# Performance work log

Hardware: AMD Instinct MI355X
Metric: run time of the kernel (lower is better)

The kernel has to match this reference:

```python
import jax, jax.numpy as jnp
import numpy as np

NUM_ANCHORS = 32
MAX_DIST = 3
DDE_ROUNDS = 2
DDE_REV_ROUNDS = 2
PE_ANCHOR_DIM = 16


def setup_inputs() -> dict:
    key = jax.random.key(0)
    ks = jax.random.split(key, 20)
    N, Ntext, NT, E, R, D, H = 20000, 19500, 500, 200000, 500, 256, 256
    PE = DDE_ROUNDS + DDE_REV_ROUNDS + PE_ANCHOR_DIM + 3
    s = 0.02
    return {
        "h_ids": jax.random.randint(ks[0], (E,), 0, N),
        "r_ids": jax.random.randint(ks[1], (E,), 0, R),
        "t_ids": jax.random.randint(ks[2], (E,), 0, N),
        "q_emb": jax.random.normal(ks[3], (D,), jnp.float32),
        "entity_embs": jax.random.normal(ks[4], (Ntext, D), jnp.float32),
        "relation_embs": jax.random.normal(ks[5], (R, D), jnp.float32),
        "topic_entity_ids": jax.random.randint(ks[6], (4,), 0, N),
        "num_entities": N,
        "num_non_text_entities": NT,
        "non_text_emb": jax.random.normal(ks[7], (1, D)) * s,
        "dist_emb": jax.random.normal(ks[8], (MAX_DIST + 2, PE_ANCHOR_DIM)) * s,
        "W_enc": jax.random.normal(ks[9], (D + PE, H)) * s,
        "b_enc": jnp.zeros((H,)),
        "gnn_W_msg": jax.random.normal(ks[10], (2, H + D, H)) * s,
        "gnn_W_gate": jax.random.normal(ks[11], (2, 2 * H, H)) * s,
        "gnn_W_upd": jax.random.normal(ks[12], (2, H, H)) * s,
        "W_out": jax.random.normal(ks[13], (H, D)) * s,
        "scorer_W1": jax.random.normal(ks[14], (4 * D + 4, H)) * s,
        "scorer_b1": jnp.zeros((H,)),
        "scorer_W2": jax.random.normal(ks[15], (H, 1)) * s,
        "scorer_b2": jnp.zeros((1,)),
    }


def reference(h_ids, r_ids, t_ids, q_emb, entity_embs, relation_embs,
              topic_entity_ids, num_entities, num_non_text_entities,
              non_text_emb, dist_emb, W_enc, b_enc,
              gnn_W_msg, gnn_W_gate, gnn_W_upd, W_out,
              scorer_W1, scorer_b1, scorer_W2, scorer_b2):
    N = num_entities
    D = q_emb.shape[0]
    E = h_ids.shape[0]
    # assemble all entity embeddings (text + broadcast non-text)
    all_emb = jnp.concatenate(
        [entity_embs, jnp.broadcast_to(non_text_emb, (num_non_text_entities, D))], axis=0)
    # anchor triple selection: question-conditioned triple scores, top-k
    qe = all_emb @ q_emb            # [N]
    qr = relation_embs @ q_emb      # [R]
    tri_score = qe[h_ids] + qr[r_ids] + qe[t_ids]  # [E]
    anchor_scores, anchor_idx = jax.lax.top_k(tri_score, NUM_ANCHORS)
    # topic DDE positional encoding (mean-aggregated label propagation)
    topic = jnp.zeros((N,), all_emb.dtype).at[topic_entity_ids].set(1.0)
    deg_t = jnp.maximum(jnp.zeros((N,)).at[t_ids].add(1.0), 1.0)
    deg_h = jnp.maximum(jnp.zeros((N,)).at[h_ids].add(1.0), 1.0)
    cols = []
    s = topic
    for _ in range(DDE_ROUNDS):
        s = jnp.zeros((N,)).at[t_ids].add(s[h_ids]) / deg_t
        cols.append(s)
    s = topic
    for _ in range(DDE_REV_ROUNDS):
        s = jnp.zeros((N,)).at[h_ids].add(s[t_ids]) / deg_h
        cols.append(s)
    pe_topic = jnp.stack(cols, axis=1)  # [N, 4]
    # anchor proximity PE: bounded BFS distance, embedded
    anchor_mask = (jnp.zeros((N,)).at[h_ids[anchor_idx]].set(1.0)
                   .at[t_ids[anchor_idx]].set(1.0))
    FAR = float(MAX_DIST + 1)
    dist = jnp.where(anchor_mask > 0, 0.0, FAR)
    for _ in range(MAX_DIST):
        c1 = jnp.full((N,), FAR).at[t_ids].min(dist[h_ids] + 1.0)
        c2 = jnp.full((N,), FAR).at[h_ids].min(dist[t_ids] + 1.0)
        dist = jnp.minimum(dist, jnp.minimum(c1, c2))
    pe_anchor = dist_emb[dist.astype(jnp.int32)]  # [N, 16]
    # path indicators (topic flag, anchor-endpoint flag, subgraph mask = full graph)
    path_ind = jnp.stack([topic, anchor_mask, jnp.ones((N,))], axis=1)
    pe_full = jnp.concatenate([pe_topic, pe_anchor, path_ind], axis=1)  # [N, 23]
    # gated GNN refine over the (full) anchor subgraph
    h = jax.nn.relu(jnp.concatenate([all_emb, pe_full], axis=1) @ W_enc + b_enc)
    rel_e = relation_embs[r_ids]  # [E, D]
    for l in range(gnn_W_msg.shape[0]):
        msg = jax.nn.relu(jnp.concatenate([h[h_ids], rel_e], axis=1) @ gnn_W_msg[l])
        agg = jnp.zeros_like(h).at[t_ids].add(msg)
        gate = jax.nn.sigmoid(jnp.concatenate([h, agg], axis=1) @ gnn_W_gate[l])
        h = h + gate * jnp.tanh(agg @ gnn_W_upd[l])
    h_final = h @ W_out  # back to emb_dim, assembled over all entities
    # scalar triple features
    is_anchor = jnp.zeros((E,)).at[anchor_idx].set(1.0)
    a_score = jnp.zeros((E,)).at[anchor_idx].set(jax.lax.stop_gradient(anchor_scores))
    scalar_feats = jnp.stack([is_anchor, a_score, topic[h_ids], topic[t_ids]], axis=1)
    # triple scorer MLP
    feats = jnp.concatenate([
        jnp.broadcast_to(q_emb, (E, D)), h_final[h_ids], rel_e,
        h_final[t_ids], scalar_feats], axis=1)  # [E, 4D+4]
    hid = jax.nn.relu(feats @ scorer_W1 + scorer_b1)
    return (hid @ scorer_W2 + scorer_b2)[:, 0]
```

## Files before the change

### kernel.cpp

```cpp
#include <hip/hip_runtime.h>
#include <math.h>

#define CDIV(a,b) (((a)+(b)-1)/(b))

typedef short short8 __attribute__((ext_vector_type(8)));
typedef float f32x4  __attribute__((ext_vector_type(4)));
typedef unsigned short u16;

__device__ __forceinline__ float warp_sum(float v){
  #pragma unroll
  for (int o=32;o;o>>=1) v += __shfl_down(v,o);
  return v;
}
__device__ __forceinline__ int warp_min(int v){
  #pragma unroll
  for (int o=32;o;o>>=1) v = min(v,__shfl_down(v,o));
  return v;
}
__device__ __forceinline__ u16 f2bf(float f){
  unsigned u = __float_as_uint(f);
  unsigned r = 0x7fffu + ((u>>16)&1u);
  return (u16)((u + r)>>16);
}
__device__ __forceinline__ float bl(u16 v){ return __uint_as_float(((unsigned)v)<<16); }

__global__ __launch_bounds__(256)
void k_rowdot_all(const float* __restrict__ ent, const float* __restrict__ nontext,
                  const float* __restrict__ q, float* __restrict__ qe,
                  int N, int Ntext,
                  const float* __restrict__ rel, float* __restrict__ qr, int R, int nb1){
  int wid = threadIdx.x>>6, lane = threadIdx.x&63;
  const float* src; float* dst; int row;
  if ((int)blockIdx.x < nb1){
    row = blockIdx.x*4 + wid; if (row >= N) return;
    src = (row < Ntext) ? (ent + (size_t)row*256) : nontext;
    dst = qe;
  } else {
    row = (blockIdx.x-nb1)*4 + wid; if (row >= R) return;
    src = rel + (size_t)row*256;
    dst = qr;
  }
  float4 a = *(const float4*)(src + lane*4);
  float4 b = *(const float4*)(q + lane*4);
  float s = a.x*b.x + a.y*b.y + a.z*b.z + a.w*b.w;
  s = warp_sum(s);
  if (!lane) dst[row] = s;
}

__global__ __launch_bounds__(256)
void k_tri(const int* __restrict__ h, const int* __restrict__ r,
           const int* __restrict__ t, const float* __restrict__ qe,
           const float* __restrict__ qr, float* __restrict__ tri,
           float* __restrict__ bmax, int* __restrict__ degh, int* __restrict__ degi, int E){
  __shared__ float red[256];
  int e = blockIdx.x*256 + threadIdx.x;
  float v = -INFINITY;
  if (e < E){
    int hh=h[e], rr=r[e], tt=t[e];
    v = qe[hh] + qr[rr] + qe[tt];
    tri[e] = v;
    atomicAdd(&degh[hh], 1);
    atomicAdd(&degi[tt], 1);
  }
  red[threadIdx.x]=v; __syncthreads();
  for (int s=128;s;s>>=1){ if ((int)threadIdx.x<s) red[threadIdx.x]=fmaxf(red[threadIdx.x],red[threadIdx.x+s]); __syncthreads(); }
  if (!threadIdx.x) bmax[blockIdx.x]=red[0];
}

__global__ __launch_bounds__(64)
void k_thresh(const float* __restrict__ bmax, float* __restrict__ thrT, int nb){
  int lane = threadIdx.x;
  float m = -INFINITY;
  for (int i=lane; i<nb; i+=64) m = fmaxf(m, bmax[i]);
  for (int it=0; it<32; it++){
    float bv = m; int bln = lane;
    #pragma unroll
    for (int o=32;o;o>>=1){
      float ov = __shfl_down(bv,o);
      int   ol = __shfl_down(bln,o);
      if (ov>bv){ bv=ov; bln=ol; }
    }
    float mv = __shfl(bv,0);
    int   wl = __shfl(bln,0);
    if (lane==wl) m = -INFINITY;
    if (it==31 && lane==0) thrT[0]=mv;
  }
}

__global__ void k_compact(const float* __restrict__ tri, const float* __restrict__ thrT,
                          int* __restrict__ cnt, int* __restrict__ ci, float* __restrict__ cv, int E){
  int e = blockIdx.x*256 + threadIdx.x; if (e>=E) return;
  float v = tri[e];
  if (v >= thrT[0]){
    int p = atomicAdd(cnt, 1);
    ci[p]=e; cv[p]=v;
  }
}

__global__ __launch_bounds__(64)
void k_final32(const int* __restrict__ ci, const float* __restrict__ cv, const int* __restrict__ cnt,
               int* __restrict__ ai, float* __restrict__ as,
               const int* __restrict__ h_ids, const int* __restrict__ t_ids,
               const int* __restrict__ topicId, int nTopic,
               float* __restrict__ topic, float* __restrict__ amask){
  int lane = threadIdx.x;
  int C = *cnt; if (C > 1024) C = 1024;
  int nIter = CDIV(C,64);
  unsigned selMask = 0;
  int myai=0; float myas=0.f;
  for (int it=0; it<32; it++){
    float bv=-INFINITY; int bi=0x7fffffff; int bj=-1;
    for (int j=0;j<nIter;j++){
      int p = lane + j*64;
      if (p < C && !((selMask>>j)&1u)){
        float v = cv[p]; int idx = ci[p];
        if (v>bv || (v==bv && idx<bi)){ bv=v; bi=idx; bj=j; }
      }
    }
    int bln = lane;
    #pragma unroll
    for (int o=32;o;o>>=1){
      float ov=__shfl_down(bv,o); int oi=__shfl_down(bi,o);
      int   oj=__shfl_down(bj,o); int ol=__shfl_down(bln,o);
      if (ov>bv || (ov==bv && oi<bi)){ bv=ov; bi=oi; bj=oj; bln=ol; }
    }
    float wv=__shfl(bv,0); int wi=__shfl(bi,0);
    int   wj=__shfl(bj,0); int wl=__shfl(bln,0);
    if (lane==wl) selMask |= (1u<<wj);
    if (lane==it){ myai=wi; myas=wv; }
  }
  if (lane<32){
    ai[lane]=myai; as[lane]=myas;
    int e = myai;
    amask[h_ids[e]]=1.f;
    amask[t_ids[e]]=1.f;
  }
  if (lane<nTopic) topic[topicId[lane]]=1.f;
}

__global__ void k_scan1(const int* __restrict__ degT, const int* __restrict__ degH,
                        int* __restrict__ offsT, int* __restrict__ offsH,
                        int* __restrict__ bsum, int N, int nb){
  __shared__ int s[256];
  int which = (int)blockIdx.x >= nb;
  int b = which ? blockIdx.x - nb : blockIdx.x;
  const int* deg = which ? degH : degT;
  int* offs = which ? offsH : offsT;
  int i = b*256 + threadIdx.x;
  int v = (i<N) ? deg[i] : 0;
  s[threadIdx.x] = v; __syncthreads();
  #pragma unroll
  for (int o=1;o<256;o<<=1){
    int add = (threadIdx.x>=(unsigned)o) ? s[threadIdx.x-o] : 0; __syncthreads();
    s[threadIdx.x] += add; __syncthreads();
  }
  if (i<N) offs[i] = s[threadIdx.x] - v;
  if (threadIdx.x==255) bsum[blockIdx.x] = s[255];
}
__global__ void k_scan2two(int* __restrict__ bsum, int nb){
  __shared__ int s[256];
  int t=threadIdx.x;
  int half = t>>7, idx = t&127;
  int v = (idx<nb)? bsum[half*nb+idx] : 0;
  s[t]=v; __syncthreads();
  #pragma unroll
  for (int o=1;o<128;o<<=1){ int add=(idx>=o)?s[t-o]:0; __syncthreads(); s[t]+=add; __syncthreads(); }
  if (idx<nb) bsum[half*nb+idx] = s[t]-v;
}
__global__ void k_scan3(int* __restrict__ offsT, int* __restrict__ offsH,
                        const int* __restrict__ bsum,
                        int* __restrict__ curT, int* __restrict__ curH, int N, int nb){
  int which = (int)blockIdx.x >= nb;
  int b = which ? blockIdx.x - nb : blockIdx.x;
  int i = b*256+threadIdx.x; if (i>=N) return;
  int* offs = which ? offsH : offsT;
  int* cur  = which ? curH  : curT;
  int o = offs[i] + bsum[blockIdx.x];
  offs[i]=o; cur[i]=o;
}
__global__ void k_place(const int* __restrict__ h, const int* __restrict__ r,
                        const int* __restrict__ t,
                        int* __restrict__ curT, int* __restrict__ curH,
                        int4* __restrict__ ehr4, int* __restrict__ etH, int E){
  int e = blockIdx.x*256+threadIdx.x; if (e>=E) return;
  int hh=h[e], tt=t[e];
  int pos = atomicAdd(&curT[tt], 1);
  ehr4[pos] = make_int4(hh, r[e], e, 0);
  int posh = atomicAdd(&curH[hh], 1);
  etH[posh] = tt;
}

__global__ __launch_bounds__(256)
void k_dde2(const int* __restrict__ offsT, const int* __restrict__ degT, const int4* __restrict__ ehr4,
            const int* __restrict__ offsH, const int* __restrict__ degH, const int* __restrict__ etH,
            const float* __restrict__ s0, const float* __restrict__ s1,
            float* __restrict__ sn0, float* __restrict__ sn1,
            float* __restrict__ pe4, int c0, int c1,
            const float* __restrict__ amask, int* __restrict__ dist0, int N){
  int wid=threadIdx.x>>6, lane=threadIdx.x&63;
  int i = blockIdx.x*4+wid; if (i>=N) return;
  int dir = blockIdx.y;
  const int* offs = dir ? offsH : offsT;
  const int* deg  = dir ? degH  : degT;
  const float* s  = dir ? s1 : s0;
  float* sn       = dir ? sn1 : sn0;
  int col         = dir ? c1 : c0;
  int start=offs[i], cnt=deg[i];
  float a=0.f;
  if (dir){
    for (int k=lane;k<cnt;k+=64) a += s[etH[start+k]];
  } else {
    for (int k=lane;k<cnt;k+=64) a += s[ehr4[start+k].x];
  }
  a = warp_sum(a);
  if (!lane){
    float v = a / fmaxf((float)cnt,1.f);
    if (sn) sn[i]=v;
    pe4[i*4+col]=v;
    if (dist0 && !dir) dist0[i] = (amask[i]>0.f)?0:4;
  }
}

__global__ __launch_bounds__(256)
void k_bfs_g(const int* __restrict__ offsT, const int* __restrict__ degT, const int4* __restrict__ ehr4,
             const int* __restrict__ offsH, const int* __restrict__ degH, const int* __restrict__ etH,
             const int* __restrict__ din, int* __restrict__ dout, int N){
  int wid=threadIdx.x>>6, lane=threadIdx.x&63;
  int i = blockIdx.x*4+wid; if (i>=N) return;
  int sT=offsT[i], cT=degT[i];
  int sH=offsH[i], cH=degH[i];
  int best = 4;
  for (int k=lane;k<cT;k+=64) best = min(best, din[ehr4[sT+k].x]+1);
  for (int k=lane;k<cH;k+=64) best = min(best, din[etH[sH+k]]+1);
  best = warp_min(best);
  if (!lane) dout[i] = min(din[i], best);
}

__global__ void k_smalls(const float* __restrict__ dist_e, const float* __restrict__ W_enc,
                         float* __restrict__ distW,
                         const float* __restrict__ nontext, float* __restrict__ encnt,
                         const float* __restrict__ q, const float* __restrict__ W1,
                         const float* __restrict__ b1, float* __restrict__ bias2){
  int b = blockIdx.x, j = threadIdx.x;
  if (b < 5){
    const float* Wpe = W_enc + (256+4)*256;
    float s=0.f;
    #pragma unroll
    for (int p=0;p<16;p++) s += dist_e[b*16+p]*Wpe[p*256+j];
    distW[b*256+j]=s;
  } else if (b == 5){
    float s=0.f;
    for (int k=0;k<256;k++) s += nontext[k]*W_enc[k*256+j];
    encnt[j]=s;
  } else {
    float s=b1[j];
    for (int k=0;k<256;k++) s += q[k]*W1[k*256+j];
    bias2[j]=s;
  }
}

__global__ __launch_bounds__(64)
void k_packall(const float* __restrict__ W_enc, const float* __restrict__ W_msg,
               const float* __restrict__ W_gate, const float* __restrict__ W_upd,
               const float* __restrict__ W1, u16* __restrict__ pbAll){
  int f = blockIdx.x, lane = threadIdx.x;
  int tgt, fid, nt16;
  if      (f < 128) { tgt=0; fid=f;      nt16=16; }
  else if (f < 256) { tgt=1; fid=f-128;  nt16=16; }
  else if (f < 384) { tgt=2; fid=f-256;  nt16=16; }
  else if (f < 896) { tgt=3; fid=f-384;  nt16=32; }
  else if (f < 1408){ tgt=4; fid=f-896;  nt16=32; }
  else if (f < 1792){ tgt=5; fid=f-1408; nt16=48; }
  else              { tgt=6; fid=f-1792; nt16=32; }
  int ks = fid/nt16, nt = fid%nt16;
  int kb = ks*32 + 8*(lane>>4);
  int n  = nt*16 + (lane&15);
  u16 v[8];
  #pragma unroll
  for (int i=0;i<8;i++){
    int k = kb+i;
    float x;
    if (tgt==0) x = W_enc[(size_t)k*256+n];
    else if (tgt==1) x = W_msg[(size_t)k*256+n];
    else if (tgt==2) x = W_msg[(size_t)(512+k)*256+n];
    else if (tgt==3 || tgt==4){
      const float* Wg = W_gate + (tgt==4 ? (size_t)512*256 : 0);
      const float* Wu = W_upd  + (tgt==4 ? (size_t)256*256 : 0);
      int blk = n>>4, c = ((blk>>1)<<4) | (n&15);
      if ((blk&1)==0) x = Wg[(size_t)k*256+c];
      else            x = (k<256) ? 0.f : Wu[(size_t)(k-256)*256+c];
    }
    else if (tgt==5){
      if (n<256)      x = W_msg[(size_t)(256+k)*256+n];
      else if (n<512) x = W_msg[(size_t)(768+k)*256+(n-256)];
      else            x = W1[(size_t)(512+k)*256+(n-512)];
    } else {
      if (n<256) x = W1[(size_t)(256+k)*256+n];
      else       x = W1[(size_t)(768+k)*256+(n-256)];
    }
    v[i]=f2bf(x);
  }
  *(uint4*)(pbAll + ((size_t)f*64+lane)*8) = *(uint4*)v;
}

__global__ __launch_bounds__(64)
void k_packf32(const float* __restrict__ W, u16* __restrict__ Bp){
  int f = blockIdx.x, lane = threadIdx.x;
  int ks = f/32, nt = f%32;
  int kb = ks*32 + 8*(lane>>4);
  int n  = nt*16 + (lane&15);
  u16 v[8];
  #pragma unroll
  for (int i=0;i<8;i++) v[i] = f2bf(W[(size_t)(kb+i)*512 + n]);
  *(uint4*)(Bp + ((size_t)f*64+lane)*8) = *(uint4*)v;
}

template<int NCOLS, int CT, int MODE, bool AF32, int MR>
__global__ __launch_bounds__(256)
void k_bgemm(const float* __restrict__ A1f, const u16* __restrict__ A2a,
             const u16* __restrict__ A2b, int K1,
             const u16* __restrict__ Bp, void* __restrict__ Cout,
             const float* __restrict__ xb, const float* __restrict__ W_enc,
             const float* __restrict__ pe4, const int* __restrict__ dist,
             const float* __restrict__ topic, const float* __restrict__ amask,
             const float* __restrict__ distW,
             int M, int K)
{
  constexpr int NT16 = NCOLS/16;
  constexpr int CPB  = NCOLS/CT;
  constexpr int NREP = CPB/32;
  const int tid  = threadIdx.x;
  const int lane = tid & 63;
  const int w    = tid >> 6;
  const int wr   = w >> 1, wc = w & 1;
  const int ct   = blockIdx.y;
  const int row0 = (blockIdx.x*2 + wr)*(16*MR);
  const int lrow = lane & 15;
  const int kc   = lane >> 4;
  int arow[MR];
  #pragma unroll
  for (int m=0;m<MR;m++){
    int rr = row0 + m*16 + lrow;
    arow[m] = (rr >= M) ? M-1 : rr;
  }

  f32x4 acc[MR][NREP];
  #pragma unroll
  for (int m=0;m<MR;m++)
    #pragma unroll
    for (int n=0;n<NREP;n++) acc[m][n] = (f32x4){0.f,0.f,0.f,0.f};

  const int ksteps = K/32;
  const int fcolBase = ct*(CPB/16) + wc*NREP;

  auto do_step = [&](short8* af, int ks){
    const u16* bp = Bp + ((size_t)(ks*NT16 + fcolBase)*64 + lane)*8;
    #pragma unroll
    for (int n=0;n<NREP;n++){
      short8 bf = *(const short8*)(bp + (size_t)n*64*8);
      #pragma unroll
      for (int m=0;m<MR;m++)
        acc[m][n] = __builtin_amdgcn_mfma_f32_16x16x32_bf16(af[m], bf, acc[m][n], 0, 0, 0);
    }
  };

  if (AF32){
    for (int ks=0; ks<ksteps; ks++){
      short8 af[MR];
      #pragma unroll
      for (int m=0;m<MR;m++){
        const float* ap = A1f + (size_t)arow[m]*256 + ks*32 + kc*8;
        float4 a0 = *(const float4*)ap;
        float4 a1 = *(const float4*)(ap+4);
        af[m][0]=(short)f2bf(a0.x); af[m][1]=(short)f2bf(a0.y); af[m][2]=(short)f2bf(a0.z); af[m][3]=(short)f2bf(a0.w);
        af[m][4]=(short)f2bf(a1.x); af[m][5]=(short)f2bf(a1.y); af[m][6]=(short)f2bf(a1.z); af[m][7]=(short)f2bf(a1.w);
      }
      do_step(af, ks);
    }
  } else {
    int s1 = K1>>5; if (s1 > ksteps) s1 = ksteps;
    for (int ks=0; ks<s1; ks++){
      short8 af[MR];
      #pragma unroll
      for (int m=0;m<MR;m++)
        af[m] = *(const short8*)(A2a + (size_t)arow[m]*256 + ks*32 + kc*8);
      do_step(af, ks);
    }
    for (int ks=s1; ks<ksteps; ks++){
      short8 af[MR];
      #pragma unroll
      for (int m=0;m<MR;m++)
        af[m] = *(const short8*)(A2b + (size_t)arow[m]*256 + (ks-s1)*32 + kc*8);
      do_step(af, ks);
    }
  }

  #pragma unroll
  for (int m=0;m<MR;m++){
    #pragma unroll
    for (int r=0;r<4;r++){
      int orow = row0 + m*16 + 4*kc + r;
      if (orow >= M) continue;
      if (MODE==0 || MODE==1){
        #pragma unroll
        for (int n=0;n<NREP;n++){
          int col = ct*CPB + wc*(CPB/2) + n*16 + lrow;
          float v = acc[m][n][r];
          if (MODE==0) ((float*)Cout)[(size_t)orow*NCOLS + col] = v;
          else         ((u16*)Cout)[(size_t)orow*NCOLS + col] = f2bf(v);
        }
      } else if (MODE==5){
        float tp = topic[orow];
        #pragma unroll
        for (int n=0;n<NREP;n++){
          int col = ct*CPB + wc*(CPB/2) + n*16 + lrow;
          float v = acc[m][n][r] + tp*xb[col];
          ((u16*)Cout)[(size_t)orow*NCOLS + col] = f2bf(v);
        }
      } else if (MODE==6){
        #pragma unroll
        for (int n=0;n<NREP;n++){
          int col = ct*CPB + wc*(CPB/2) + n*16 + lrow;
          float v = acc[m][n][r];
          if (col >= 512) v += xb[col-512];
          ((u16*)Cout)[(size_t)orow*NCOLS + col] = f2bf(v);
        }
      } else if (MODE==3){
        float p0=pe4[orow*4+0], p1=pe4[orow*4+1], p2=pe4[orow*4+2], p3=pe4[orow*4+3];
        int dd=dist[orow];
        float tp=topic[orow], am=amask[orow];
        const float* Wpe = W_enc + 256*256;
        #pragma unroll
        for (int n=0;n<NREP;n++){
          int col = ct*CPB + wc*(CPB/2) + n*16 + lrow;
          float v = acc[m][n][r];
          v += xb[col] + Wpe[22*256+col]
             + p0*Wpe[col] + p1*Wpe[256+col] + p2*Wpe[512+col] + p3*Wpe[768+col]
             + distW[dd*256+col] + tp*Wpe[20*256+col] + am*Wpe[21*256+col];
          ((u16*)Cout)[(size_t)orow*256 + col] = f2bf(fmaxf(v, 0.f));
        }
      } else {
        #pragma unroll
        for (int k=0;k<NREP/2;k++){
          int col = (ct*(CPB/32) + wc*(CPB/64) + k)*16 + lrow;
          size_t idx = (size_t)orow*256 + col;
          float g = 1.f/(1.f+expf(-acc[m][2*k][r]));
          float u = tanhf(acc[m][2*k+1][r]);
          float v = bl(A2a[idx]) + g*u;
          ((u16*)Cout)[idx] = f2bf(v);
        }
      }
    }
  }
}

__global__ __launch_bounds__(256)
void k_encnt_fill(const float* __restrict__ encnt, const float* __restrict__ b_enc,
                  const float* __restrict__ W_enc, const float* __restrict__ pe4,
                  const int* __restrict__ dist, const float* __restrict__ topic,
                  const float* __restrict__ amask, const float* __restrict__ distW,
                  u16* __restrict__ hB, int Ntext){
  int i = Ntext + blockIdx.x, j = threadIdx.x;
  const float* Wpe = W_enc + 256*256;
  float p0=pe4[i*4+0], p1=pe4[i*4+1], p2=pe4[i*4+2], p3=pe4[i*4+3];
  int d = dist[i];
  float tp = topic[i], am = amask[i];
  float v = encnt[j] + b_enc[j] + Wpe[22*256+j]
          + p0*Wpe[j] + p1*Wpe[256+j] + p2*Wpe[512+j] + p3*Wpe[768+j]
          + distW[d*256+j] + tp*Wpe[20*256+j] + am*Wpe[21*256+j];
  hB[(size_t)i*256+j] = f2bf(fmaxf(v, 0.f));
}

__global__ __launch_bounds__(256)
void k_agg(const int* __restrict__ offs, const int* __restrict__ degi,
           const int4* __restrict__ ehr4,
           const u16* __restrict__ hm, const u16* __restrict__ relC, int colOff,
           u16* __restrict__ agg, int N){
  int wid = threadIdx.x>>6, lane = threadIdx.x&63;
  int i = blockIdx.x*4 + wid; if (i>=N) return;
  int start = offs[i], cnt = degi[i];
  int c4 = lane*4;
  float a0=0.f,a1=0.f,a2=0.f,a3=0.f;
  int k=0;
  for (; k+3<cnt; k+=4){
    int4 hr[4]; uint2 ua[4], ub[4];
    #pragma unroll
    for (int j=0;j<4;j++) hr[j] = ehr4[start+k+j];
    #pragma unroll
    for (int j=0;j<4;j++){
      ua[j] = *(const uint2*)(hm + (size_t)hr[j].x*256 + c4);
      ub[j] = *(const uint2*)(relC + (size_t)hr[j].y*768 + colOff + c4);
    }
    #pragma unroll
    for (int j=0;j<4;j++){
      a0 += fmaxf(bl((u16)(ua[j].x&0xffff))+bl((u16)(ub[j].x&0xffff)),0.f);
      a1 += fmaxf(bl((u16)(ua[j].x>>16))  +bl((u16)(ub[j].x>>16)),  0.f);
      a2 += fmaxf(bl((u16)(ua[j].y&0xffff))+bl((u16)(ub[j].y&0xffff)),0.f);
      a3 += fmaxf(bl((u16)(ua[j].y>>16))  +bl((u16)(ub[j].y>>16)),  0.f);
    }
  }
  for (; k<cnt; k++){
    int4 hr = ehr4[start+k];
    uint2 ua = *(const uint2*)(hm + (size_t)hr.x*256 + c4);
    uint2 ub = *(const uint2*)(relC + (size_t)hr.y*768 + colOff + c4);
    a0 += fmaxf(bl((u16)(ua.x&0xffff))+bl((u16)(ub.x&0xffff)),0.f);
    a1 += fmaxf(bl((u16)(ua.x>>16))  +bl((u16)(ub.x>>16)),  0.f);
    a2 += fmaxf(bl((u16)(ua.y&0xffff))+bl((u16)(ub.y&0xffff)),0.f);
    a3 += fmaxf(bl((u16)(ua.y>>16))  +bl((u16)(ub.y>>16)),  0.f);
  }
  uint2 o;
  o.x = (unsigned)f2bf(a0) | ((unsigned)f2bf(a1)<<16);
  o.y = (unsigned)f2bf(a2) | ((unsigned)f2bf(a3)<<16);
  *(uint2*)(agg + (size_t)i*256 + c4) = o;
}

__global__ __launch_bounds__(256)
void k_score(const int* __restrict__ offs, const int* __restrict__ degi,
             const int4* __restrict__ ehr4,
             const u16* __restrict__ UHT, const u16* __restrict__ relC,
             const float* __restrict__ W2,
             const float* __restrict__ b2, float* __restrict__ out, int N){
  int wid = threadIdx.x>>6, lane = threadIdx.x&63;
  int i = blockIdx.x*4 + wid; if (i>=N) return;
  int start = offs[i], cnt = degi[i];
  if (!cnt) return;
  int c = lane*4;
  uint2 ud = *(const uint2*)(UHT + (size_t)i*512 + 256 + c);
  float b0 = bl((u16)(ud.x&0xffff)), b1v = bl((u16)(ud.x>>16));
  float b2v= bl((u16)(ud.y&0xffff)), b3  = bl((u16)(ud.y>>16));
  float4 w = *(const float4*)(W2 + c);
  float bout = b2[0];
  int k=0;
  for (; k+3<cnt; k+=4){
    int4 e[4]; uint2 ua[4], ub[4];
    #pragma unroll
    for (int j=0;j<4;j++) e[j] = ehr4[start+k+j];
    #pragma unroll
    for (int j=0;j<4;j++){
      ua[j] = *(const uint2*)(UHT + (size_t)e[j].x*512 + c);
      ub[j] = *(const uint2*)(relC + (size_t)e[j].y*768 + 512 + c);
    }
    float p[4];
    #pragma unroll
    for (int j=0;j<4;j++){
      p[j] = fmaxf(b0 + bl((u16)(ua[j].x&0xffff)) + bl((u16)(ub[j].x&0xffff)),0.f)*w.x
           + fmaxf(b1v+ bl((u16)(ua[j].x>>16))    + bl((u16)(ub[j].x>>16)),  0.f)*w.y
           + fmaxf(b2v+ bl((u16)(ua[j].y&0xffff)) + bl((u16)(ub[j].y&0xffff)),0.f)*w.z
           + fmaxf(b3 + bl((u16)(ua[j].y>>16))    + bl((u16)(ub[j].y>>16)),  0.f)*w.w;
    }
    #pragma unroll
    for (int j=0;j<4;j++) p[j] = warp_sum(p[j]);
    if (!lane){
      #pragma unroll
      for (int j=0;j<4;j++) out[e[j].z] = p[j] + bout;
    }
  }
  for (; k<cnt; k++){
    int4 e0 = ehr4[start+k];
    uint2 ua = *(const uint2*)(UHT + (size_t)e0.x*512 + c);
    uint2 ub = *(const uint2*)(relC + (size_t)e0.y*768 + 512 + c);
    float p = fmaxf(b0 + bl((u16)(ua.x&0xffff)) + bl((u16)(ub.x&0xffff)),0.f)*w.x
            + fmaxf(b1v+ bl((u16)(ua.x>>16))    + bl((u16)(ub.x>>16)),  0.f)*w.y
            + fmaxf(b2v+ bl((u16)(ua.y&0xffff)) + bl((u16)(ub.y&0xffff)),0.f)*w.z
            + fmaxf(b3 + bl((u16)(ua.y>>16))    + bl((u16)(ub.y>>16)),  0.f)*w.w;
    p = warp_sum(p);
    if (!lane) out[e0.z] = p + bout;
  }
}

__global__ __launch_bounds__(256)
void k_patch(const int* __restrict__ ai, const float* __restrict__ as,
             const int* __restrict__ h_ids, const int* __restrict__ r_ids, const int* __restrict__ t_ids,
             const u16* __restrict__ UHT, const u16* __restrict__ relC,
             const float* __restrict__ W1s, const float* __restrict__ W2,
             const float* __restrict__ b2, float* __restrict__ out){
  int wid = threadIdx.x>>6, lane = threadIdx.x&63;
  int k = blockIdx.x*4 + wid; if (k>=32) return;
  int e = ai[k];
  int h=h_ids[e], r=r_ids[e], t=t_ids[e];
  float aS = as[k];
  int c = lane*4;
  uint2 ua = *(const uint2*)(UHT + (size_t)h*512 + c);
  uint2 ud = *(const uint2*)(UHT + (size_t)t*512 + 256 + c);
  uint2 ub = *(const uint2*)(relC + (size_t)r*768 + 512 + c);
  float4 w0 = *(const float4*)(W1s + 0*256 + c);
  float4 w1 = *(const float4*)(W1s + 1*256 + c);
  float4 acc;
  acc.x = bl((u16)(ua.x&0xffff))+bl((u16)(ub.x&0xffff))+bl((u16)(ud.x&0xffff)) + w0.x + aS*w1.x;
  acc.y = bl((u16)(ua.x>>16))  +bl((u16)(ub.x>>16))  +bl((u16)(ud.x>>16))   + w0.y + aS*w1.y;
  acc.z = bl((u16)(ua.y&0xffff))+bl((u16)(ub.y&0xffff))+bl((u16)(ud.y&0xffff)) + w0.z + aS*w1.z;
  acc.w = bl((u16)(ua.y>>16))  +bl((u16)(ub.y>>16))  +bl((u16)(ud.y>>16))   + w0.w + aS*w1.w;
  acc.x=fmaxf(acc.x,0.f); acc.y=fmaxf(acc.y,0.f); acc.z=fmaxf(acc.z,0.f); acc.w=fmaxf(acc.w,0.f);
  float4 w = *(const float4*)(W2 + c);
  float p = acc.x*w.x + acc.y*w.y + acc.z*w.z + acc.w*w.w;
  p = warp_sum(p);
  if (!lane) out[e] = p + b2[0];
}

extern "C" void kernel_launch(void* const* d_in, const int* in_sizes, int n_in,
                              void* d_out, int out_size, void* d_ws, size_t ws_size,
                              hipStream_t stream)
{
  const int*   h_ids   = (const int*)d_in[0];
  const int*   r_ids   = (const int*)d_in[1];
  const int*   t_ids   = (const int*)d_in[2];
  const float* q       = (const float*)d_in[3];
  const float* ent     = (const float*)d_in[4];
  const float* rel     = (const float*)d_in[5];
  const int*   topicId = (const int*)d_in[6];
  const float* nontext = (const float*)d_in[9];
  const float* dist_e  = (const float*)d_in[10];
  const float* W_enc   = (const float*)d_in[11];
  const float* b_enc   = (const float*)d_in[12];
  const float* W_msg   = (const float*)d_in[13];
  const float* W_gate  = (const float*)d_in[14];
  const float* W_upd   = (const float*)d_in[15];
  const float* W_out   = (const float*)d_in[16];
  const float* W1      = (const float*)d_in[17];
  const float* b1      = (const float*)d_in[18];
  const float* W2      = (const float*)d_in[19];
  const float* b2      = (const float*)d_in[20];
  float* out = (float*)d_out;

  const int E = in_sizes[0];
  const int Ntext = in_sizes[4]/256;
  const int R = in_sizes[5]/256;
  const int NT = 500;
  const int N = Ntext + NT;
  const int nTopic = in_sizes[6];
  const int BIGK1 = 1<<28;

  char* ws = (char*)d_ws;
  size_t off = 0;
  auto alloc = [&](size_t bytes)->void*{
    size_t o = (off + 255) & ~(size_t)255;
    off = o + bytes;
    return (void*)(ws + o);
  };
  u16*   hB1   = (u16*)  alloc((size_t)N*256*2);
  u16*   hB2   = (u16*)  alloc((size_t)N*256*2);
  u16*   hmB   = (u16*)  alloc((size_t)N*256*2);
  u16*   aggB  = (u16*)  alloc((size_t)N*256*2);
  u16*   relC  = (u16*)  alloc((size_t)R*768*2);
  u16*   UHT   = (u16*)  alloc((size_t)N*512*2);
  float* WcombF= (float*)alloc((size_t)256*512*4);
  u16*   pbWcomb=(u16*)  alloc((size_t)256*512*2);
  float* qe    = (float*)alloc((size_t)N*4);
  float* qr    = (float*)alloc((size_t)R*4);
  float* tri   = (float*)alloc((size_t)E*4);
  float* bmax  = (float*)alloc(1024*4);
  float* thrT  = (float*)alloc(4);
  int*   ci    = (int*)  alloc((size_t)E*4);
  float* cv    = (float*)alloc((size_t)E*4);
  int*   ai    = (int*)  alloc(32*4);
  float* as    = (float*)alloc(32*4);
  float* pe4   = (float*)alloc((size_t)N*16);
  int*   dA    = (int*)  alloc((size_t)N*4);
  int*   dB    = (int*)  alloc((size_t)N*4);
  float* distW = (float*)alloc(5*256*4);
  float* encnt = (float*)alloc(256*4);
  float* bias2 = (float*)alloc(256*4);
  int*   offsT = (int*)  alloc((size_t)N*4);
  int*   offsH = (int*)  alloc((size_t)N*4);
  int*   bsum  = (int*)  alloc(256*4);
  int*   curT  = (int*)  alloc((size_t)N*4);
  int*   curH  = (int*)  alloc((size_t)N*4);
  int4*  ehr4  = (int4*) alloc((size_t)E*16);
  int*   etH   = (int*)  alloc((size_t)E*4);
  float* sA    = (float*)alloc((size_t)N*4);
  float* sB    = (float*)alloc((size_t)N*4);
  u16*   pbAll = (u16*)  alloc((size_t)2048*512*2);
  int*   cnt   = (int*)  alloc(4);
  float* topic = (float*)alloc((size_t)N*4);
  float* amask = (float*)alloc((size_t)N*4);
  int*   deghI = (int*)  alloc((size_t)N*4);
  int*   degiI = (int*)  alloc((size_t)N*4);
  (void)ws_size; (void)n_in; (void)out_size;

  size_t zbytes = (char*)(degiI + N) - (char*)cnt;
  hipMemsetAsync(cnt, 0, zbytes, stream);

  u16* pbWenc = pbAll + (size_t)0*512;
  u16* pbWmT0 = pbAll + (size_t)128*512;
  u16* pbWmT1 = pbAll + (size_t)256*512;
  u16* pbGU0  = pbAll + (size_t)384*512;
  u16* pbGU1  = pbAll + (size_t)896*512;
  u16* pbRelC = pbAll + (size_t)1408*512;
  u16* pbW1ht = pbAll + (size_t)1792*512;

  const float* tW = W1 + (size_t)(1024+2)*256;

  k_packall<<<2048,64,0,stream>>>(W_enc, W_msg, W_gate, W_upd, W1, pbAll);
  k_bgemm<512,8,0,true,1><<<dim3(8,8),256,0,stream>>>(W_out, nullptr, nullptr, BIGK1, pbW1ht, WcombF,
      nullptr,nullptr,nullptr,nullptr,nullptr,nullptr,nullptr, 256, 256);
  k_packf32<<<256,64,0,stream>>>(WcombF, pbWcomb);

  int nb1 = CDIV(N,4);
  k_rowdot_all<<<nb1+CDIV(R,4),256,0,stream>>>(ent, nontext, q, qe, N, Ntext, rel, qr, R, nb1);
  int nbE = CDIV(E,256);
  k_tri<<<nbE,256,0,stream>>>(h_ids, r_ids, t_ids, qe, qr, tri, bmax, deghI, degiI, E);
  k_thresh<<<1,64,0,stream>>>(bmax, thrT, nbE);
  k_compact<<<nbE,256,0,stream>>>(tri, thrT, cnt, ci, cv, E);
  k_final32<<<1,64,0,stream>>>(ci, cv, cnt, ai, as, h_ids, t_ids, topicId, nTopic, topic, amask);

  int nb = CDIV(N,256);
  k_scan1<<<2*nb,256,0,stream>>>(degiI, deghI, offsT, offsH, bsum, N, nb);
  k_scan2two<<<1,256,0,stream>>>(bsum, nb);
  k_scan3<<<2*nb,256,0,stream>>>(offsT, offsH, bsum, curT, curH, N, nb);
  k_place<<<nbE,256,0,stream>>>(h_ids, r_ids, t_ids, curT, curH, ehr4, etH, E);

  int nbN4 = CDIV(N,4);
  k_dde2<<<dim3(nbN4,2),256,0,stream>>>(offsT, degiI, ehr4, offsH, deghI, etH,
      topic, topic, sB, sA, pe4, 0, 2, nullptr, nullptr, N);
  k_dde2<<<dim3(nbN4,2),256,0,stream>>>(offsT, degiI, ehr4, offsH, deghI, etH,
      sB, sA, nullptr, nullptr, pe4, 1, 3, amask, dA, N);

  k_bfs_g<<<nbN4,256,0,stream>>>(offsT, degiI, ehr4, offsH, deghI, etH, dA, dB, N);
  k_bfs_g<<<nbN4,256,0,stream>>>(offsT, degiI, ehr4, offsH, deghI, etH, dB, dA, N);
  k_bfs_g<<<nbN4,256,0,stream>>>(offsT, degiI, ehr4, offsH, deghI, etH, dA, dB, N);

  k_smalls<<<7,256,0,stream>>>(dist_e, W_enc, distW, nontext, encnt, q, W1, b1, bias2);

  k_bgemm<768,6,6,true,1><<<dim3(CDIV(R,32),6),256,0,stream>>>(rel, nullptr, nullptr, BIGK1, pbRelC, relC,
      bias2,nullptr,nullptr,nullptr,nullptr,nullptr,nullptr, R, 256);

  k_bgemm<256,4,3,true,2><<<dim3(CDIV(Ntext,64),4),256,0,stream>>>(ent, nullptr, nullptr, BIGK1, pbWenc, hB1,
      b_enc, W_enc, pe4, dB, topic, amask, distW, Ntext, 256);
  k_encnt_fill<<<N-Ntext,256,0,stream>>>(encnt, b_enc, W_enc, pe4, dB, topic, amask, distW, hB1, Ntext);

  for (int l=0;l<2;l++){
    const u16* pT = l ? pbWmT1 : pbWmT0;
    const u16* pGU = l ? pbGU1 : pbGU0;
    u16* hinB  = l ? hB2 : hB1;
    u16* houtB = l ? hB1 : hB2;
    k_bgemm<256,4,1,false,2><<<dim3(CDIV(N,64),4),256,0,stream>>>(nullptr, hinB, nullptr, BIGK1, pT, hmB,
        nullptr,nullptr,nullptr,nullptr,nullptr,nullptr,nullptr, N, 256);
    k_agg<<<CDIV(N,4),256,0,stream>>>(offsT, degiI, ehr4, hmB, relC, l*256, aggB, N);
    k_bgemm<512,4,4,false,2><<<dim3(CDIV(N,64),4),256,0,stream>>>(nullptr, hinB, aggB, 256, pGU, houtB,
        nullptr,nullptr,nullptr,nullptr,nullptr,nullptr,nullptr, N, 512);
  }

  k_bgemm<512,4,5,false,2><<<dim3(CDIV(N,64),4),256,0,stream>>>(nullptr, hB1, nullptr, BIGK1, pbWcomb, UHT,
      tW,nullptr,nullptr,nullptr,topic,nullptr,nullptr, N, 256);

  k_score<<<CDIV(N,4),256,0,stream>>>(offsT, degiI, ehr4, UHT, relC, W2, b2, out, N);
  k_patch<<<8,256,0,stream>>>(ai, as, h_ids, r_ids, t_ids, UHT, relC,
                              W1+(size_t)1024*256, W2, b2, out);
}
```

Measured before the change: 402.5 us.

## Split edge records into int2 pairs plus separate index, widen GEMM column tiles

The CSR edge array changes from int4 (head, relation, edge id, pad) to an int2 (head, relation) array plus a separate edge-index array. The gather kernels (dde, bfs, agg, score) then read half as many bytes per edge, and only the score kernel reads the edge index. Separately, the bgemm launches switch from 4 to 2 column blocks via a template parameter, which gives each block a wider output tile but launches fewer blocks per GEMM.

```diff
diff --git a/kernel.cpp b/kernel.cpp
--- a/kernel.cpp
+++ b/kernel.cpp
@@ -181,17 +181,19 @@
 __global__ void k_place(const int* __restrict__ h, const int* __restrict__ r,
                         const int* __restrict__ t,
                         int* __restrict__ curT, int* __restrict__ curH,
-                        int4* __restrict__ ehr4, int* __restrict__ etH, int E){
+                        int2* __restrict__ ehr, int* __restrict__ eIdx,
+                        int* __restrict__ etH, int E){
   int e = blockIdx.x*256+threadIdx.x; if (e>=E) return;
   int hh=h[e], tt=t[e];
   int pos = atomicAdd(&curT[tt], 1);
-  ehr4[pos] = make_int4(hh, r[e], e, 0);
+  ehr[pos] = make_int2(hh, r[e]);
+  eIdx[pos] = e;
   int posh = atomicAdd(&curH[hh], 1);
   etH[posh] = tt;
 }
 
 __global__ __launch_bounds__(256)
-void k_dde2(const int* __restrict__ offsT, const int* __restrict__ degT, const int4* __restrict__ ehr4,
+void k_dde2(const int* __restrict__ offsT, const int* __restrict__ degT, const int2* __restrict__ ehr,
             const int* __restrict__ offsH, const int* __restrict__ degH, const int* __restrict__ etH,
             const float* __restrict__ s0, const float* __restrict__ s1,
             float* __restrict__ sn0, float* __restrict__ sn1,
@@ -210,7 +212,7 @@
   if (dir){
     for (int k=lane;k<cnt;k+=64) a += s[etH[start+k]];
   } else {
-    for (int k=lane;k<cnt;k+=64) a += s[ehr4[start+k].x];
+    for (int k=lane;k<cnt;k+=64) a += s[ehr[start+k].x];
   }
   a = warp_sum(a);
   if (!lane){
@@ -222,7 +224,7 @@
 }
 
 __global__ __launch_bounds__(256)
-void k_bfs_g(const int* __restrict__ offsT, const int* __restrict__ degT, const int4* __restrict__ ehr4,
+void k_bfs_g(const int* __restrict__ offsT, const int* __restrict__ degT, const int2* __restrict__ ehr,
              const int* __restrict__ offsH, const int* __restrict__ degH, const int* __restrict__ etH,
              const int* __restrict__ din, int* __restrict__ dout, int N){
   int wid=threadIdx.x>>6, lane=threadIdx.x&63;
@@ -230,7 +232,7 @@
   int sT=offsT[i], cT=degT[i];
   int sH=offsH[i], cH=degH[i];
   int best = 4;
-  for (int k=lane;k<cT;k+=64) best = min(best, din[ehr4[sT+k].x]+1);
+  for (int k=lane;k<cT;k+=64) best = min(best, din[ehr[sT+k].x]+1);
   for (int k=lane;k<cH;k+=64) best = min(best, din[etH[sH+k]]+1);
   best = warp_min(best);
   if (!lane) dout[i] = min(din[i], best);
@@ -473,7 +475,7 @@
 
 __global__ __launch_bounds__(256)
 void k_agg(const int* __restrict__ offs, const int* __restrict__ degi,
-           const int4* __restrict__ ehr4,
+           const int2* __restrict__ ehr,
            const u16* __restrict__ hm, const u16* __restrict__ relC, int colOff,
            u16* __restrict__ agg, int N){
   int wid = threadIdx.x>>6, lane = threadIdx.x&63;
@@ -483,9 +485,9 @@
   float a0=0.f,a1=0.f,a2=0.f,a3=0.f;
   int k=0;
   for (; k+3<cnt; k+=4){
-    int4 hr[4]; uint2 ua[4], ub[4];
-    #pragma unroll
-    for (int j=0;j<4;j++) hr[j] = ehr4[start+k+j];
+    int2 hr[4]; uint2 ua[4], ub[4];
+    #pragma unroll
+    for (int j=0;j<4;j++) hr[j] = ehr[start+k+j];
     #pragma unroll
     for (int j=0;j<4;j++){
       ua[j] = *(const uint2*)(hm + (size_t)hr[j].x*256 + c4);
@@ -500,7 +502,7 @@
     }
   }
   for (; k<cnt; k++){
-    int4 hr = ehr4[start+k];
+    int2 hr = ehr[start+k];
     uint2 ua = *(const uint2*)(hm + (size_t)hr.x*256 + c4);
     uint2 ub = *(const uint2*)(relC + (size_t)hr.y*768 + colOff + c4);
     a0 += fmaxf(bl((u16)(ua.x&0xffff))+bl((u16)(ub.x&0xffff)),0.f);
@@ -516,7 +518,7 @@
 
 __global__ __launch_bounds__(256)
 void k_score(const int* __restrict__ offs, const int* __restrict__ degi,
-             const int4* __restrict__ ehr4,
+             const int2* __restrict__ ehr, const int* __restrict__ eIdx,
              const u16* __restrict__ UHT, const u16* __restrict__ relC,
              const float* __restrict__ W2,
              const float* __restrict__ b2, float* __restrict__ out, int N){
@@ -532,9 +534,9 @@
   float bout = b2[0];
   int k=0;
   for (; k+3<cnt; k+=4){
-    int4 e[4]; uint2 ua[4], ub[4];
-    #pragma unroll
-    for (int j=0;j<4;j++) e[j] = ehr4[start+k+j];
+    int2 e[4]; uint2 ua[4], ub[4];
+    #pragma unroll
+    for (int j=0;j<4;j++) e[j] = ehr[start+k+j];
     #pragma unroll
     for (int j=0;j<4;j++){
       ua[j] = *(const uint2*)(UHT + (size_t)e[j].x*512 + c);
@@ -552,11 +554,11 @@
     for (int j=0;j<4;j++) p[j] = warp_sum(p[j]);
     if (!lane){
       #pragma unroll
-      for (int j=0;j<4;j++) out[e[j].z] = p[j] + bout;
+      for (int j=0;j<4;j++) out[eIdx[start+k+j]] = p[j] + bout;
     }
   }
   for (; k<cnt; k++){
-    int4 e0 = ehr4[start+k];
+    int2 e0 = ehr[start+k];
     uint2 ua = *(const uint2*)(UHT + (size_t)e0.x*512 + c);
     uint2 ub = *(const uint2*)(relC + (size_t)e0.y*768 + 512 + c);
     float p = fmaxf(b0 + bl((u16)(ua.x&0xffff)) + bl((u16)(ub.x&0xffff)),0.f)*w.x
@@ -564,7 +566,7 @@
             + fmaxf(b2v+ bl((u16)(ua.y&0xffff)) + bl((u16)(ub.y&0xffff)),0.f)*w.z
             + fmaxf(b3 + bl((u16)(ua.y>>16))    + bl((u16)(ub.y>>16)),  0.f)*w.w;
     p = warp_sum(p);
-    if (!lane) out[e0.z] = p + bout;
+    if (!lane) out[eIdx[start+k]] = p + bout;
   }
 }
 
@@ -665,7 +667,8 @@
   int*   bsum  = (int*)  alloc(256*4);
   int*   curT  = (int*)  alloc((size_t)N*4);
   int*   curH  = (int*)  alloc((size_t)N*4);
-  int4*  ehr4  = (int4*) alloc((size_t)E*16);
+  int2*  ehr   = (int2*) alloc((size_t)E*8);
+  int*   eIdx  = (int*)  alloc((size_t)E*4);
   int*   etH   = (int*)  alloc((size_t)E*4);
   float* sA    = (float*)alloc((size_t)N*4);
   float* sB    = (float*)alloc((size_t)N*4);
@@ -707,24 +710,24 @@
   k_scan1<<<2*nb,256,0,stream>>>(degiI, deghI, offsT, offsH, bsum, N, nb);
   k_scan2two<<<1,256,0,stream>>>(bsum, nb);
   k_scan3<<<2*nb,256,0,stream>>>(offsT, offsH, bsum, curT, curH, N, nb);
-  k_place<<<nbE,256,0,stream>>>(h_ids, r_ids, t_ids, curT, curH, ehr4, etH, E);
+  k_place<<<nbE,256,0,stream>>>(h_ids, r_ids, t_ids, curT, curH, ehr, eIdx, etH, E);
 
   int nbN4 = CDIV(N,4);
-  k_dde2<<<dim3(nbN4,2),256,0,stream>>>(offsT, degiI, ehr4, offsH, deghI, etH,
+  k_dde2<<<dim3(nbN4,2),256,0,stream>>>(offsT, degiI, ehr, offsH, deghI, etH,
       topic, topic, sB, sA, pe4, 0, 2, nullptr, nullptr, N);
-  k_dde2<<<dim3(nbN4,2),256,0,stream>>>(offsT, degiI, ehr4, offsH, deghI, etH,
+  k_dde2<<<dim3(nbN4,2),256,0,stream>>>(offsT, degiI, ehr, offsH, deghI, etH,
       sB, sA, nullptr, nullptr, pe4, 1, 3, amask, dA, N);
 
-  k_bfs_g<<<nbN4,256,0,stream>>>(offsT, degiI, ehr4, offsH, deghI, etH, dA, dB, N);
-  k_bfs_g<<<nbN4,256,0,stream>>>(offsT, degiI, ehr4, offsH, deghI, etH, dB, dA, N);
-  k_bfs_g<<<nbN4,256,0,stream>>>(offsT, degiI, ehr4, offsH, deghI, etH, dA, dB, N);
+  k_bfs_g<<<nbN4,256,0,stream>>>(offsT, degiI, ehr, offsH, deghI, etH, dA, dB, N);
+  k_bfs_g<<<nbN4,256,0,stream>>>(offsT, degiI, ehr, offsH, deghI, etH, dB, dA, N);
+  k_bfs_g<<<nbN4,256,0,stream>>>(offsT, degiI, ehr, offsH, deghI, etH, dA, dB, N);
 
   k_smalls<<<7,256,0,stream>>>(dist_e, W_enc, distW, nontext, encnt, q, W1, b1, bias2);
 
   k_bgemm<768,6,6,true,1><<<dim3(CDIV(R,32),6),256,0,stream>>>(rel, nullptr, nullptr, BIGK1, pbRelC, relC,
       bias2,nullptr,nullptr,nullptr,nullptr,nullptr,nullptr, R, 256);
 
-  k_bgemm<256,4,3,true,2><<<dim3(CDIV(Ntext,64),4),256,0,stream>>>(ent, nullptr, nullptr, BIGK1, pbWenc, hB1,
+  k_bgemm<256,2,3,true,2><<<dim3(CDIV(Ntext,64),2),256,0,stream>>>(ent, nullptr, nullptr, BIGK1, pbWenc, hB1,
       b_enc, W_enc, pe4, dB, topic, amask, distW, Ntext, 256);
   k_encnt_fill<<<N-Ntext,256,0,stream>>>(encnt, b_enc, W_enc, pe4, dB, topic, amask, distW, hB1, Ntext);
 
@@ -733,17 +736,17 @@
     const u16* pGU = l ? pbGU1 : pbGU0;
     u16* hinB  = l ? hB2 : hB1;
     u16* houtB = l ? hB1 : hB2;
-    k_bgemm<256,4,1,false,2><<<dim3(CDIV(N,64),4),256,0,stream>>>(nullptr, hinB, nullptr, BIGK1, pT, hmB,
+    k_bgemm<256,2,1,false,2><<<dim3(CDIV(N,64),2),256,0,stream>>>(nullptr, hinB, nullptr, BIGK1, pT, hmB,
         nullptr,nullptr,nullptr,nullptr,nullptr,nullptr,nullptr, N, 256);
-    k_agg<<<CDIV(N,4),256,0,stream>>>(offsT, degiI, ehr4, hmB, relC, l*256, aggB, N);
-    k_bgemm<512,4,4,false,2><<<dim3(CDIV(N,64),4),256,0,stream>>>(nullptr, hinB, aggB, 256, pGU, houtB,
+    k_agg<<<CDIV(N,4),256,0,stream>>>(offsT, degiI, ehr, hmB, relC, l*256, aggB, N);
+    k_bgemm<512,2,4,false,2><<<dim3(CDIV(N,64),2),256,0,stream>>>(nullptr, hinB, aggB, 256, pGU, houtB,
         nullptr,nullptr,nullptr,nullptr,nullptr,nullptr,nullptr, N, 512);
   }
 
-  k_bgemm<512,4,5,false,2><<<dim3(CDIV(N,64),4),256,0,stream>>>(nullptr, hB1, nullptr, BIGK1, pbWcomb, UHT,
+  k_bgemm<512,2,5,false,2><<<dim3(CDIV(N,64),2),256,0,stream>>>(nullptr, hB1, nullptr, BIGK1, pbWcomb, UHT,
       tW,nullptr,nullptr,nullptr,topic,nullptr,nullptr, N, 256);
 
-  k_score<<<CDIV(N,4),256,0,stream>>>(offsT, degiI, ehr4, UHT, relC, W2, b2, out, N);
+  k_score<<<CDIV(N,4),256,0,stream>>>(offsT, degiI, ehr, eIdx, UHT, relC, W2, b2, out, N);
   k_patch<<<8,256,0,stream>>>(ai, as, h_ids, r_ids, t_ids, UHT, relC,
                               W1+(size_t)1024*256, W2, b2, out);
 }
```

Result: faster. 384.2 us, median of 2 (-4.5%).
